# Kernel optimization log

Hardware: AMD Instinct MI355X
Metric: run time of the kernel (lower is better)

Reference implementation:

```python
import jax, jax.numpy as jnp
import numpy as np


def setup_inputs() -> dict:
    key = jax.random.key(0)
    k1, k2 = jax.random.split(key)
    B, N, M = 8, 8192, 8192
    pred = jax.random.normal(k1, (B, N, 3), dtype=jnp.float32)
    target = jax.random.normal(k2, (B, M, 3), dtype=jnp.float32)
    return {"pred": pred, "target": target}


def reference(pred, target):
    # pairwise squared distances: (B, N, M)
    pred_sq = jnp.sum(pred ** 2, axis=2, keepdims=True)            # (B, N, 1)
    target_sq = jnp.sum(target ** 2, axis=2, keepdims=True)        # (B, M, 1)
    dist = pred_sq + jnp.swapaxes(target_sq, 1, 2) \
           - 2.0 * jnp.einsum('bnd,bmd->bnm', pred, target)
    dist = jnp.maximum(dist, 0.0)
    cd_p2t = jnp.mean(jnp.min(dist, axis=2))   # pred -> target
    cd_t2p = jnp.mean(jnp.min(dist, axis=1))   # target -> pred (bidirectional=True)
    return cd_p2t + cd_t2p
```

## Files before the change

kernel.cpp:

```cpp
#include <hip/hip_runtime.h>
#include <math.h>

#define THREADS  256
#define NPTS     8192
#define BATCH    8
#define ENTRIES  (2 * BATCH * NPTS)
#define ENC_U4   (2 * BATCH * 8 * 2048)
#define ENC_BYTES ((size_t)ENC_U4 * 16)
#define NPLANES  4
#define MINS_BYTES ((size_t)NPLANES * ENTRIES * 4)
#define WS1_BYTES (ENC_BYTES + MINS_BYTES)
#define WS_BYTES  ((size_t)ENTRIES * 4)

typedef __attribute__((ext_vector_type(8)))  short bf16x8;
typedef __attribute__((ext_vector_type(16))) float f32x16;

union FragCast { uint4 u; bf16x8 v; };

__device__ __forceinline__ unsigned short f2bf(float f) {
    unsigned u = __float_as_uint(f);
    unsigned r = (u + 0x7FFFu + ((u >> 16) & 1u)) >> 16;
    return (unsigned short)r;
}
__device__ __forceinline__ float bf2f(unsigned short h) {
    return __uint_as_float(((unsigned)h) << 16);
}
#define PK(a, b) (((unsigned)(a)) | (((unsigned)(b)) << 16))
#define BF_ONE 0x3F80u

__device__ __forceinline__ void encode_db_point(float x, float y, float z,
                                                uint4& h0, uint4& h1) {
    const float sq = fmaf(x, x, fmaf(y, y, z * z));
    const unsigned short xh = f2bf(x), yh = f2bf(y), zh = f2bf(z);
    const unsigned short xl = f2bf(x - bf2f(xh));
    const unsigned short yl = f2bf(y - bf2f(yh));
    const unsigned short zl = f2bf(z - bf2f(zh));
    const unsigned short sh = f2bf(sq);
    const unsigned short sl = f2bf(sq - bf2f(sh));
    h0 = make_uint4(PK(xh, yh), PK(zh, xl), PK(yl, zl), PK(xh, yh));
    h1 = make_uint4(PK(zh, xl), PK(yl, zl), PK(sh, sl), PK(BF_ONE, BF_ONE));
}

__global__ __launch_bounds__(THREADS)
void chamfer_encode_kernel(const float* __restrict__ pred,
                           const float* __restrict__ target,
                           uint4* __restrict__ enc,
                           float* __restrict__ out)
{
    const int t   = blockIdx.x * THREADS + threadIdx.x;
    if (t == 0) out[0] = 0.0f;
    const int arr = t >> 16;
    const int rem = t & 0xFFFF;
    const int b   = rem >> 13;
    const int p   = rem & (NPTS - 1);
    const float* src = (arr ? target : pred) + ((size_t)b * NPTS + p) * 3;
    uint4 h0, h1;
    encode_db_point(src[0], src[1], src[2], h0, h1);
    const int T = p >> 5, c = p & 31;
    uint4* base = enc + (size_t)(arr * BATCH + b) * 16384;
    base[T * 64 + c]      = h0;
    base[T * 64 + c + 32] = h1;
}

__global__ __launch_bounds__(THREADS, 4)
void chamfer_mfma4_kernel(const float* __restrict__ pred,
                          const float* __restrict__ target,
                          const uint4* __restrict__ enc,
                          float* __restrict__ mins)
{
    const int bx  = blockIdx.x;
    const int ds  = bx & 3;
    const int qb  = (bx >> 2) & 31;
    const int b   = (bx >> 7) & 7;
    const int dir = bx >> 10;

    const float* qarr = dir ? target : pred;
    const int arr_db  = dir ^ 1;

    const int tid  = threadIdx.x;
    const int ln   = tid & 63;
    const int w    = tid >> 6;
    const int half = ln >> 5;

    bf16x8 bq0, bq1;
    const int qbase = qb * 256 + w * 64;
    #pragma unroll
    for (int nb = 0; nb < 2; ++nb) {
        const int qi = qbase + nb * 32 + (ln & 31);
        const float* qp = qarr + ((size_t)b * NPTS + qi) * 3;
        const float x = qp[0], y = qp[1], z = qp[2];
        const float sq = fmaf(x, x, fmaf(y, y, z * z));
        const float wx = -2.0f * x, wy = -2.0f * y, wz = -2.0f * z;
        const unsigned short wxh = f2bf(wx), wyh = f2bf(wy), wzh = f2bf(wz);
        const unsigned short wxl = f2bf(wx - bf2f(wxh));
        const unsigned short wyl = f2bf(wy - bf2f(wyh));
        const unsigned short wzl = f2bf(wz - bf2f(wzh));
        const unsigned short sh  = f2bf(sq);
        const unsigned short sl  = f2bf(sq - bf2f(sh));
        FragCast fc;
        if (half == 0) fc.u = make_uint4(PK(wxh, wyh), PK(wzh, wxh), PK(wyh, wzh), PK(wxl, wyl));
        else           fc.u = make_uint4(PK(wzl, wxl), PK(wyl, wzl), PK(BF_ONE, BF_ONE), PK(sh, sl));
        if (nb == 0) bq0 = fc.v; else bq1 = fc.v;
    }

    const f32x16 zacc = {};
    f32x16 m0, m1;
    #pragma unroll
    for (int i = 0; i < 16; ++i) { m0[i] = INFINITY; m1[i] = INFINITY; }

    const uint4* gbase = enc + (size_t)(arr_db * BATCH + b) * 16384 + ds * 4096 + ln;

    #pragma unroll 2
    for (int jj = 0; jj < 64; jj += 2) {
        FragCast a0, a1;
        a0.u = gbase[jj * 64];
        a1.u = gbase[jj * 64 + 64];
        const f32x16 c00 = __builtin_amdgcn_mfma_f32_32x32x16_bf16(a0.v, bq0, zacc, 0, 0, 0);
        const f32x16 c01 = __builtin_amdgcn_mfma_f32_32x32x16_bf16(a1.v, bq0, zacc, 0, 0, 0);
        #pragma unroll
        for (int i = 0; i < 16; ++i)
            m0[i] = fminf(fminf(m0[i], c00[i]), c01[i]);
        const f32x16 c10 = __builtin_amdgcn_mfma_f32_32x32x16_bf16(a0.v, bq1, zacc, 0, 0, 0);
        const f32x16 c11 = __builtin_amdgcn_mfma_f32_32x32x16_bf16(a1.v, bq1, zacc, 0, 0, 0);
        #pragma unroll
        for (int i = 0; i < 16; ++i)
            m1[i] = fminf(fminf(m1[i], c10[i]), c11[i]);
    }

    float r0, r1;
    {
        float a0 = fminf(fminf(m0[0], m0[1]), fminf(m0[2], m0[3]));
        float a1 = fminf(fminf(m0[4], m0[5]), fminf(m0[6], m0[7]));
        float a2 = fminf(fminf(m0[8], m0[9]), fminf(m0[10], m0[11]));
        float a3 = fminf(fminf(m0[12], m0[13]), fminf(m0[14], m0[15]));
        r0 = fminf(fminf(a0, a1), fminf(a2, a3));
        float b0 = fminf(fminf(m1[0], m1[1]), fminf(m1[2], m1[3]));
        float b1 = fminf(fminf(m1[4], m1[5]), fminf(m1[6], m1[7]));
        float b2 = fminf(fminf(m1[8], m1[9]), fminf(m1[10], m1[11]));
        float b3 = fminf(fminf(m1[12], m1[13]), fminf(m1[14], m1[15]));
        r1 = fminf(fminf(b0, b1), fminf(b2, b3));
    }
    r0 = fminf(r0, __shfl_xor(r0, 32, 64));
    r1 = fminf(r1, __shfl_xor(r1, 32, 64));
    if (ln < 32) {
        const int base = ds * ENTRIES + dir * (BATCH * NPTS) + b * NPTS + qbase;
        mins[base + ln]      = r0;
        mins[base + 32 + ln] = r1;
    }
}

__global__ __launch_bounds__(THREADS)
void chamfer_finish4_kernel(const float* __restrict__ mins,
                            float* __restrict__ out,
                            float inv_count)
{
    const int t = blockIdx.x * THREADS + threadIdx.x;
    const float4* p0 = (const float4*)mins;
    const float4* p1 = (const float4*)(mins + ENTRIES);
    const float4* p2 = (const float4*)(mins + 2 * ENTRIES);
    const float4* p3 = (const float4*)(mins + 3 * ENTRIES);
    const float4 a = p0[t], c = p1[t], d = p2[t], e = p3[t];
    float s = fmaxf(fminf(fminf(a.x, c.x), fminf(d.x, e.x)), 0.0f)
            + fmaxf(fminf(fminf(a.y, c.y), fminf(d.y, e.y)), 0.0f)
            + fmaxf(fminf(fminf(a.z, c.z), fminf(d.z, e.z)), 0.0f)
            + fmaxf(fminf(fminf(a.w, c.w), fminf(d.w, e.w)), 0.0f);
    float v = s;
    #pragma unroll
    for (int off = 32; off > 0; off >>= 1)
        v += __shfl_down(v, off, 64);
    __shared__ float wsum[THREADS / 64];
    if ((threadIdx.x & 63) == 0) wsum[threadIdx.x >> 6] = v;
    __syncthreads();
    if (threadIdx.x == 0)
        atomicAdd(out, (wsum[0] + wsum[1] + wsum[2] + wsum[3]) * inv_count);
}

__global__ __launch_bounds__(THREADS, 4)
void chamfer_mfma_kernel(const float* __restrict__ pred,
                         const float* __restrict__ target,
                         unsigned* __restrict__ wskeys)
{
    __shared__ short lds[32 * 64 * 8];
    const int bx  = blockIdx.x;
    const int ds  = bx & 3;
    const int qb  = (bx >> 2) & 15;
    const int b   = (bx >> 6) & 7;
    const int dir = bx >> 9;
    const float* qarr = dir ? target : pred;
    const float* darr = dir ? pred   : target;
    const int tid  = threadIdx.x;
    const int ln   = tid & 63;
    const int w    = tid >> 6;
    const int half = ln >> 5;

    bf16x8 bq[4];
    const int qbase = qb * 512 + w * 128;
    #pragma unroll
    for (int nb = 0; nb < 4; ++nb) {
        const int qi = qbase + nb * 32 + (ln & 31);
        const float* qp = qarr + ((size_t)b * NPTS + qi) * 3;
        const float x = qp[0], y = qp[1], z = qp[2];
        const float sq = fmaf(x, x, fmaf(y, y, z * z));
        const float wx = -2.0f * x, wy = -2.0f * y, wz = -2.0f * z;
        const unsigned short wxh = f2bf(wx), wyh = f2bf(wy), wzh = f2bf(wz);
        const unsigned short wxl = f2bf(wx - bf2f(wxh));
        const unsigned short wyl = f2bf(wy - bf2f(wyh));
        const unsigned short wzl = f2bf(wz - bf2f(wzh));
        const unsigned short sh  = f2bf(sq);
        const unsigned short sl  = f2bf(sq - bf2f(sh));
        FragCast fc;
        if (half == 0) fc.u = make_uint4(PK(wxh, wyh), PK(wzh, wxh), PK(wyh, wzh), PK(wxl, wyl));
        else           fc.u = make_uint4(PK(wzl, wxl), PK(wyl, wzl), PK(BF_ONE, BF_ONE), PK(sh, sl));
        bq[nb] = fc.v;
    }

    float mn[4] = {INFINITY, INFINITY, INFINITY, INFINITY};
    const int range0 = ds * 2048;
    for (int chunk = 0; chunk < 2; ++chunk) {
        #pragma unroll
        for (int it = 0; it < 4; ++it) {
            const int pl = it * THREADS + tid;
            const int p  = range0 + chunk * 1024 + pl;
            const float* tp = darr + ((size_t)b * NPTS + p) * 3;
            uint4 h0, h1;
            encode_db_point(tp[0], tp[1], tp[2], h0, h1);
            const int j = pl >> 5, c = pl & 31;
            *(uint4*)&lds[(j * 64 + c) * 8]      = h0;
            *(uint4*)&lds[(j * 64 + c + 32) * 8] = h1;
        }
        __syncthreads();
        #pragma unroll 4
        for (int j = 0; j < 32; ++j) {
            const bf16x8 a = *(const bf16x8*)&lds[(j * 64 + ln) * 8];
            f32x16 z = {};
            f32x16 c0 = __builtin_amdgcn_mfma_f32_32x32x16_bf16(a, bq[0], z, 0, 0, 0);
            f32x16 c1 = __builtin_amdgcn_mfma_f32_32x32x16_bf16(a, bq[1], z, 0, 0, 0);
            f32x16 c2 = __builtin_amdgcn_mfma_f32_32x32x16_bf16(a, bq[2], z, 0, 0, 0);
            f32x16 c3 = __builtin_amdgcn_mfma_f32_32x32x16_bf16(a, bq[3], z, 0, 0, 0);
            #pragma unroll
            for (int i = 0; i < 16; i += 2) {
                mn[0] = fminf(mn[0], fminf(c0[i], c0[i + 1]));
                mn[1] = fminf(mn[1], fminf(c1[i], c1[i + 1]));
                mn[2] = fminf(mn[2], fminf(c2[i], c2[i + 1]));
                mn[3] = fminf(mn[3], fminf(c3[i], c3[i + 1]));
            }
        }
        __syncthreads();
    }
    const int obase = dir * (BATCH * NPTS) + b * NPTS;
    #pragma unroll
    for (int nb = 0; nb < 4; ++nb) {
        const float o = __shfl_xor(mn[nb], 32, 64);
        const float m = fminf(mn[nb], o);
        if (ln < 32) {
            const unsigned u   = __float_as_uint(m);
            const unsigned key = (u >> 31) ? ~u : (u | 0x80000000u);
            atomicMin(&wskeys[obase + qbase + nb * 32 + ln], key);
        }
    }
}

__global__ __launch_bounds__(THREADS)
void chamfer_finish_kernel(const unsigned* __restrict__ ws,
                           float* __restrict__ out,
                           float inv_count)
{
    const int t = blockIdx.x * THREADS + threadIdx.x;
    const uint4 kk = ((const uint4*)ws)[t];
    float s = 0.0f;
    { const unsigned u = (kk.x >> 31) ? (kk.x ^ 0x80000000u) : ~kk.x; s += fmaxf(__uint_as_float(u), 0.0f); }
    { const unsigned u = (kk.y >> 31) ? (kk.y ^ 0x80000000u) : ~kk.y; s += fmaxf(__uint_as_float(u), 0.0f); }
    { const unsigned u = (kk.z >> 31) ? (kk.z ^ 0x80000000u) : ~kk.z; s += fmaxf(__uint_as_float(u), 0.0f); }
    { const unsigned u = (kk.w >> 31) ? (kk.w ^ 0x80000000u) : ~kk.w; s += fmaxf(__uint_as_float(u), 0.0f); }
    float v = s;
    #pragma unroll
    for (int off = 32; off > 0; off >>= 1)
        v += __shfl_down(v, off, 64);
    __shared__ float wsum[THREADS / 64];
    if ((threadIdx.x & 63) == 0) wsum[threadIdx.x >> 6] = v;
    __syncthreads();
    if (threadIdx.x == 0)
        atomicAdd(out, (wsum[0] + wsum[1] + wsum[2] + wsum[3]) * inv_count);
}

__global__ __launch_bounds__(THREADS, 2)
void chamfer_fallback_kernel(const float* __restrict__ pred,
                             const float* __restrict__ target,
                             float* __restrict__ out,
                             float inv_count)
{
    __shared__ float4 lds[2048];
    const float* q  = (blockIdx.y == 0) ? pred   : target;
    const float* db = (blockIdx.y == 0) ? target : pred;
    const int b = blockIdx.x / (NPTS / THREADS);
    const int n = (blockIdx.x % (NPTS / THREADS)) * THREADS + threadIdx.x;
    const float* qp = q + ((size_t)b * NPTS + n) * 3;
    const float px = qp[0], py = qp[1], pz = qp[2];
    const float npx = -2.0f * px, npy = -2.0f * py, npz = -2.0f * pz;
    const float P = px * px + py * py + pz * pz;
    const float* dbB = db + (size_t)b * NPTS * 3;
    float m0 = INFINITY;
    for (int c0 = 0; c0 < NPTS; c0 += 2048) {
        for (int k = 0; k < 2048 / THREADS; ++k) {
            const int j = k * THREADS + threadIdx.x;
            const float* tp = dbB + (size_t)(c0 + j) * 3;
            const float tx = tp[0], ty = tp[1], tz = tp[2];
            lds[j] = make_float4(tx, ty, tz, tx * tx + ty * ty + tz * tz);
        }
        __syncthreads();
        for (int j = 0; j < 2048; ++j) {
            const float4 T = lds[j];
            m0 = fminf(m0, fmaf(npx, T.x, fmaf(npy, T.y, fmaf(npz, T.z, T.w))));
        }
        __syncthreads();
    }
    float v = fmaxf(P + m0, 0.0f);
    #pragma unroll
    for (int off = 32; off > 0; off >>= 1)
        v += __shfl_down(v, off, 64);
    __shared__ float wsum[THREADS / 64];
    if ((threadIdx.x & 63) == 0) wsum[threadIdx.x >> 6] = v;
    __syncthreads();
    if (threadIdx.x == 0)
        atomicAdd(out, (wsum[0] + wsum[1] + wsum[2] + wsum[3]) * inv_count);
}

extern "C" void kernel_launch(void* const* d_in, const int* in_sizes, int n_in,
                              void* d_out, int out_size, void* d_ws, size_t ws_size,
                              hipStream_t stream) {
    const float* pred   = (const float*)d_in[0];
    const float* target = (const float*)d_in[1];
    float* out = (float*)d_out;
    const float inv_count = 1.0f / (float)(BATCH * NPTS);

    if (ws_size >= WS1_BYTES) {
        uint4* enc  = (uint4*)d_ws;
        float* mins = (float*)((char*)d_ws + ENC_BYTES);
        chamfer_encode_kernel<<<(2 * BATCH * NPTS) / THREADS, THREADS, 0, stream>>>(
            pred, target, enc, out);
        chamfer_mfma4_kernel<<<2048, THREADS, 0, stream>>>(pred, target, enc, mins);
        chamfer_finish4_kernel<<<ENTRIES / (THREADS * 4), THREADS, 0, stream>>>(
            mins, out, inv_count);
    } else if (ws_size >= WS_BYTES) {
        hipMemsetAsync(out, 0, out_size * sizeof(float), stream);
        unsigned* ws = (unsigned*)d_ws;
        hipMemsetAsync(ws, 0xFF, WS_BYTES, stream);
        chamfer_mfma_kernel<<<1024, THREADS, 0, stream>>>(pred, target, ws);
        chamfer_finish_kernel<<<ENTRIES / (THREADS * 4), THREADS, 0, stream>>>(ws, out, inv_count);
    } else {
        hipMemsetAsync(out, 0, out_size * sizeof(float), stream);
        dim3 grid(BATCH * (NPTS / THREADS), 2);
        chamfer_fallback_kernel<<<grid, THREADS, 0, stream>>>(pred, target, out, inv_count);
    }
}
```

Before: 95.42 us.

## Reuse each database fragment across four query tiles in MFMA kernel

The MFMA kernel now has each wave handle 128 queries (four B fragments) instead of 64, so every global load of an encoded database fragment feeds four MFMAs rather than two. The grid is halved to 1024 blocks to match, and the running minima are kept as 8-wide vectors by folding pairs of MFMA outputs, which keeps register use roughly flat. The aim is to cut global/L2 load traffic per MFMA and the per-block query setup cost. In exchange there are fewer blocks to spread across the CUs, and each wave runs a longer dependent loop.

```diff
diff --git a/kernel.cpp b/kernel.cpp
--- a/kernel.cpp
+++ b/kernel.cpp
@@ -13,6 +13,7 @@
 #define WS_BYTES  ((size_t)ENTRIES * 4)
 
 typedef __attribute__((ext_vector_type(8)))  short bf16x8;
+typedef __attribute__((ext_vector_type(8)))  float f32x8;
 typedef __attribute__((ext_vector_type(16))) float f32x16;
 
 union FragCast { uint4 u; bf16x8 v; };
@@ -39,6 +40,22 @@
     const unsigned short sl = f2bf(sq - bf2f(sh));
     h0 = make_uint4(PK(xh, yh), PK(zh, xl), PK(yl, zl), PK(xh, yh));
     h1 = make_uint4(PK(zh, xl), PK(yl, zl), PK(sh, sl), PK(BF_ONE, BF_ONE));
+}
+
+__device__ __forceinline__ bf16x8 make_query_frag(const float* qp, int half) {
+    const float x = qp[0], y = qp[1], z = qp[2];
+    const float sq = fmaf(x, x, fmaf(y, y, z * z));
+    const float wx = -2.0f * x, wy = -2.0f * y, wz = -2.0f * z;
+    const unsigned short wxh = f2bf(wx), wyh = f2bf(wy), wzh = f2bf(wz);
+    const unsigned short wxl = f2bf(wx - bf2f(wxh));
+    const unsigned short wyl = f2bf(wy - bf2f(wyh));
+    const unsigned short wzl = f2bf(wz - bf2f(wzh));
+    const unsigned short sh  = f2bf(sq);
+    const unsigned short sl  = f2bf(sq - bf2f(sh));
+    FragCast fc;
+    if (half == 0) fc.u = make_uint4(PK(wxh, wyh), PK(wzh, wxh), PK(wyh, wzh), PK(wxl, wyl));
+    else           fc.u = make_uint4(PK(wzl, wxl), PK(wyl, wzl), PK(BF_ONE, BF_ONE), PK(sh, sl));
+    return fc.v;
 }
 
 __global__ __launch_bounds__(THREADS)
@@ -70,9 +87,9 @@
 {
     const int bx  = blockIdx.x;
     const int ds  = bx & 3;
-    const int qb  = (bx >> 2) & 31;
-    const int b   = (bx >> 7) & 7;
-    const int dir = bx >> 10;
+    const int qb  = (bx >> 2) & 15;
+    const int b   = (bx >> 6) & 7;
+    const int dir = bx >> 9;
 
     const float* qarr = dir ? target : pred;
     const int arr_db  = dir ^ 1;
@@ -82,70 +99,46 @@
     const int w    = tid >> 6;
     const int half = ln >> 5;
 
-    bf16x8 bq0, bq1;
-    const int qbase = qb * 256 + w * 64;
-    #pragma unroll
-    for (int nb = 0; nb < 2; ++nb) {
-        const int qi = qbase + nb * 32 + (ln & 31);
-        const float* qp = qarr + ((size_t)b * NPTS + qi) * 3;
-        const float x = qp[0], y = qp[1], z = qp[2];
-        const float sq = fmaf(x, x, fmaf(y, y, z * z));
-        const float wx = -2.0f * x, wy = -2.0f * y, wz = -2.0f * z;
-        const unsigned short wxh = f2bf(wx), wyh = f2bf(wy), wzh = f2bf(wz);
-        const unsigned short wxl = f2bf(wx - bf2f(wxh));
-        const unsigned short wyl = f2bf(wy - bf2f(wyh));
-        const unsigned short wzl = f2bf(wz - bf2f(wzh));
-        const unsigned short sh  = f2bf(sq);
-        const unsigned short sl  = f2bf(sq - bf2f(sh));
-        FragCast fc;
-        if (half == 0) fc.u = make_uint4(PK(wxh, wyh), PK(wzh, wxh), PK(wyh, wzh), PK(wxl, wyl));
-        else           fc.u = make_uint4(PK(wzl, wxl), PK(wyl, wzl), PK(BF_ONE, BF_ONE), PK(sh, sl));
-        if (nb == 0) bq0 = fc.v; else bq1 = fc.v;
-    }
+    const int qbase = qb * 512 + w * 128;
+    const size_t qrow = (size_t)b * NPTS;
+    bf16x8 bq0 = make_query_frag(qarr + (qrow + qbase +  0 + (ln & 31)) * 3, half);
+    bf16x8 bq1 = make_query_frag(qarr + (qrow + qbase + 32 + (ln & 31)) * 3, half);
+    bf16x8 bq2 = make_query_frag(qarr + (qrow + qbase + 64 + (ln & 31)) * 3, half);
+    bf16x8 bq3 = make_query_frag(qarr + (qrow + qbase + 96 + (ln & 31)) * 3, half);
 
     const f32x16 zacc = {};
-    f32x16 m0, m1;
-    #pragma unroll
-    for (int i = 0; i < 16; ++i) { m0[i] = INFINITY; m1[i] = INFINITY; }
+    f32x8 m0, m1, m2, m3;
+    #pragma unroll
+    for (int i = 0; i < 8; ++i) { m0[i] = INFINITY; m1[i] = INFINITY; m2[i] = INFINITY; m3[i] = INFINITY; }
 
     const uint4* gbase = enc + (size_t)(arr_db * BATCH + b) * 16384 + ds * 4096 + ln;
 
     #pragma unroll 2
-    for (int jj = 0; jj < 64; jj += 2) {
-        FragCast a0, a1;
-        a0.u = gbase[jj * 64];
-        a1.u = gbase[jj * 64 + 64];
-        const f32x16 c00 = __builtin_amdgcn_mfma_f32_32x32x16_bf16(a0.v, bq0, zacc, 0, 0, 0);
-        const f32x16 c01 = __builtin_amdgcn_mfma_f32_32x32x16_bf16(a1.v, bq0, zacc, 0, 0, 0);
-        #pragma unroll
-        for (int i = 0; i < 16; ++i)
-            m0[i] = fminf(fminf(m0[i], c00[i]), c01[i]);
-        const f32x16 c10 = __builtin_amdgcn_mfma_f32_32x32x16_bf16(a0.v, bq1, zacc, 0, 0, 0);
-        const f32x16 c11 = __builtin_amdgcn_mfma_f32_32x32x16_bf16(a1.v, bq1, zacc, 0, 0, 0);
-        #pragma unroll
-        for (int i = 0; i < 16; ++i)
-            m1[i] = fminf(fminf(m1[i], c10[i]), c11[i]);
-    }
-
-    float r0, r1;
-    {
-        float a0 = fminf(fminf(m0[0], m0[1]), fminf(m0[2], m0[3]));
-        float a1 = fminf(fminf(m0[4], m0[5]), fminf(m0[6], m0[7]));
-        float a2 = fminf(fminf(m0[8], m0[9]), fminf(m0[10], m0[11]));
-        float a3 = fminf(fminf(m0[12], m0[13]), fminf(m0[14], m0[15]));
-        r0 = fminf(fminf(a0, a1), fminf(a2, a3));
-        float b0 = fminf(fminf(m1[0], m1[1]), fminf(m1[2], m1[3]));
-        float b1 = fminf(fminf(m1[4], m1[5]), fminf(m1[6], m1[7]));
-        float b2 = fminf(fminf(m1[8], m1[9]), fminf(m1[10], m1[11]));
-        float b3 = fminf(fminf(m1[12], m1[13]), fminf(m1[14], m1[15]));
-        r1 = fminf(fminf(b0, b1), fminf(b2, b3));
-    }
-    r0 = fminf(r0, __shfl_xor(r0, 32, 64));
-    r1 = fminf(r1, __shfl_xor(r1, 32, 64));
-    if (ln < 32) {
-        const int base = ds * ENTRIES + dir * (BATCH * NPTS) + b * NPTS + qbase;
-        mins[base + ln]      = r0;
-        mins[base + 32 + ln] = r1;
+    for (int jj = 0; jj < 64; ++jj) {
+        FragCast a;
+        a.u = gbase[jj * 64];
+        const f32x16 c0 = __builtin_amdgcn_mfma_f32_32x32x16_bf16(a.v, bq0, zacc, 0, 0, 0);
+        #pragma unroll
+        for (int i = 0; i < 8; ++i) m0[i] = fminf(fminf(m0[i], c0[2*i]), c0[2*i+1]);
+        const f32x16 c1 = __builtin_amdgcn_mfma_f32_32x32x16_bf16(a.v, bq1, zacc, 0, 0, 0);
+        #pragma unroll
+        for (int i = 0; i < 8; ++i) m1[i] = fminf(fminf(m1[i], c1[2*i]), c1[2*i+1]);
+        const f32x16 c2 = __builtin_amdgcn_mfma_f32_32x32x16_bf16(a.v, bq2, zacc, 0, 0, 0);
+        #pragma unroll
+        for (int i = 0; i < 8; ++i) m2[i] = fminf(fminf(m2[i], c2[2*i]), c2[2*i+1]);
+        const f32x16 c3 = __builtin_amdgcn_mfma_f32_32x32x16_bf16(a.v, bq3, zacc, 0, 0, 0);
+        #pragma unroll
+        for (int i = 0; i < 8; ++i) m3[i] = fminf(fminf(m3[i], c3[2*i]), c3[2*i+1]);
+    }
+
+    const int base = ds * ENTRIES + dir * (BATCH * NPTS) + b * NPTS + qbase;
+    #pragma unroll
+    for (int nb = 0; nb < 4; ++nb) {
+        const f32x8& m = (nb == 0) ? m0 : (nb == 1) ? m1 : (nb == 2) ? m2 : m3;
+        float r = fminf(fminf(fminf(m[0], m[1]), fminf(m[2], m[3])),
+                        fminf(fminf(m[4], m[5]), fminf(m[6], m[7])));
+        r = fminf(r, __shfl_xor(r, 32, 64));
+        if (ln < 32) mins[base + nb * 32 + ln] = r;
     }
 }
 
@@ -196,23 +189,8 @@
     bf16x8 bq[4];
     const int qbase = qb * 512 + w * 128;
     #pragma unroll
-    for (int nb = 0; nb < 4; ++nb) {
-        const int qi = qbase + nb * 32 + (ln & 31);
-        const float* qp = qarr + ((size_t)b * NPTS + qi) * 3;
-        const float x = qp[0], y = qp[1], z = qp[2];
-        const float sq = fmaf(x, x, fmaf(y, y, z * z));
-        const float wx = -2.0f * x, wy = -2.0f * y, wz = -2.0f * z;
-        const unsigned short wxh = f2bf(wx), wyh = f2bf(wy), wzh = f2bf(wz);
-        const unsigned short wxl = f2bf(wx - bf2f(wxh));
-        const unsigned short wyl = f2bf(wy - bf2f(wyh));
-        const unsigned short wzl = f2bf(wz - bf2f(wzh));
-        const unsigned short sh  = f2bf(sq);
-        const unsigned short sl  = f2bf(sq - bf2f(sh));
-        FragCast fc;
-        if (half == 0) fc.u = make_uint4(PK(wxh, wyh), PK(wzh, wxh), PK(wyh, wzh), PK(wxl, wyl));
-        else           fc.u = make_uint4(PK(wzl, wxl), PK(wyl, wzl), PK(BF_ONE, BF_ONE), PK(sh, sl));
-        bq[nb] = fc.v;
-    }
+    for (int nb = 0; nb < 4; ++nb)
+        bq[nb] = make_query_frag(qarr + ((size_t)b * NPTS + qbase + nb * 32 + (ln & 31)) * 3, half);
 
     float mn[4] = {INFINITY, INFINITY, INFINITY, INFINITY};
     const int range0 = ds * 2048;
@@ -338,7 +316,7 @@
         float* mins = (float*)((char*)d_ws + ENC_BYTES);
         chamfer_encode_kernel<<<(2 * BATCH * NPTS) / THREADS, THREADS, 0, stream>>>(
             pred, target, enc, out);
-        chamfer_mfma4_kernel<<<2048, THREADS, 0, stream>>>(pred, target, enc, mins);
+        chamfer_mfma4_kernel<<<1024, THREADS, 0, stream>>>(pred, target, enc, mins);
         chamfer_finish4_kernel<<<ENTRIES / (THREADS * 4), THREADS, 0, stream>>>(
             mins, out, inv_count);
     } else if (ws_size >= WS_BYTES) {
```

Result: no change. 94.58 us (-0.9%).
